# Performance work log

Hardware: AMD Instinct MI355X
Metric: run time of the kernel (lower is better)

The kernel has to match this reference:

```python
import jax, jax.numpy as jnp
import numpy as np

EPS = 1e-12  # F.normalize eps


def setup_inputs() -> dict:
    key = jax.random.key(0)
    ks = jax.random.split(key, 3)
    B, C, D, R = 4096, 32, 128, 8
    return {
        "source": jax.random.normal(ks[0], (B, C, D), dtype=jnp.float32),
        "data": jax.random.normal(ks[1], (B, C, D), dtype=jnp.float32),
        "W": jax.random.normal(ks[2], (R, D, D), dtype=jnp.float32) * (1.0 / np.sqrt(D)),
        "a": jnp.ones((R, C, D), dtype=jnp.float32),
        "c": jnp.ones((R, C, D), dtype=jnp.float32),
        "d": jnp.zeros((R, C, D), dtype=jnp.float32),
    }


def reference(source, data, W, a, c, d):
    # Generate all reflection directions in one batched GEMM:
    # Linear(bias=False): x @ W_r^T, W_r is [out, in]
    v = jnp.einsum("bci,roi->rbco", source, W)          # [R, B, C, D]
    # DynamicTanh: tanh(a*x)*c + d, params [R, C, D] broadcast over batch
    v = jnp.tanh(a[:, None] * v) * c[:, None] + d[:, None]
    # F.normalize(p=2, dim=-1) with eps clamp
    norm = jnp.linalg.norm(v, axis=-1, keepdims=True)
    v = v / jnp.maximum(norm, EPS)

    # Sequential Householder reflections H_R(...H_2(H_1(x)))
    def step(x, vec):
        dot = jnp.sum(vec * x, axis=-1, keepdims=True)  # [B, C, 1]
        return x - 2.0 * vec * dot, None

    out, _ = jax.lax.scan(step, data, v)
    return out
```

## Files before the change

### kernel.cpp

```cpp
#include <hip/hip_runtime.h>
#include <stdint.h>

#define B_DIM 4096
#define C_DIM 32
#define D_DIM 128
#define R_DIM 8
#define BM    128
#define NTHREADS 256

typedef __bf16 bf16x8 __attribute__((ext_vector_type(8)));
typedef float  f32x4  __attribute__((ext_vector_type(4)));

__device__ __forceinline__ uint32_t f2bf(float f) {
  uint32_t u = __float_as_uint(f);
  return (u + 0x7FFFu + ((u >> 16) & 1u)) >> 16;
}

#if __has_builtin(__builtin_amdgcn_exp2f)
#define EXP2F(x) __builtin_amdgcn_exp2f(x)
#else
#define EXP2F(x) exp2f(x)
#endif
#if __has_builtin(__builtin_amdgcn_rcpf)
#define RCPF(x) __builtin_amdgcn_rcpf(x)
#else
#define RCPF(x) (1.0f / (x))
#endif

__device__ __forceinline__ void load_lds16(const void* g, void* l) {
  __builtin_amdgcn_global_load_lds(
      (const __attribute__((address_space(1))) uint32_t*)g,
      (__attribute__((address_space(3))) uint32_t*)l, 16, 0, 0);
}

template <int CTRL>
__device__ __forceinline__ float ror_add(float v) {
  int r = __builtin_amdgcn_update_dpp(0, __builtin_bit_cast(int, v), CTRL, 0xf, 0xf, true);
  return v + __builtin_bit_cast(float, r);
}
__device__ __forceinline__ float red16(float v) {
  v = ror_add<0x128>(v);
  v = ror_add<0x124>(v);
  v = ror_add<0x122>(v);
  v = ror_add<0x121>(v);
  return v;
}

__global__ void prep_w(const float* __restrict__ W, uint32_t* __restrict__ ws) {
  uint32_t t = blockIdx.x * 256u + threadIdx.x;
  uint32_t c  = t >> 2;
  uint32_t j  = t & 3u;
  uint32_t ln = c & 63u;
  uint32_t kt = (c >> 6) & 3u;
  uint32_t n  = (c >> 8) & 7u;
  uint32_t r  = c >> 11;
  uint32_t o  = n * 16u + (ln & 15u);
  uint32_t k  = kt * 32u + (ln >> 4) * 8u + j * 2u;
  const float2 w2 = *reinterpret_cast<const float2*>(
      W + ((size_t)(r * 128u + o)) * 128u + k);
  ws[t] = f2bf(w2.x) | (f2bf(w2.y) << 16);
}

__global__ void prep_acd(const float* __restrict__ A, const float* __restrict__ C,
                         const float* __restrict__ D, float* __restrict__ o) {
  uint32_t t = blockIdx.x * 256u + threadIdx.x;
  uint32_t col = t & 127u, r = (t >> 7) & 7u, c = t >> 10;
  uint32_t in = (r * 32u + c) * 128u + col;
  float av = A[in], cv = C[in], dv = D[in];
  float4 v = make_float4(av * 2.88539008177793f,
                         -2.f * cv, cv + dv, 0.f);
  *reinterpret_cast<float4*>(o + (size_t)t * 4u) = v;
}

__global__ __launch_bounds__(NTHREADS, 2)
void rot_kernel(const float* __restrict__ src, const float* __restrict__ data,
                const uint8_t* __restrict__ wsw, const float* __restrict__ wacd,
                float* __restrict__ out)
{
  __shared__ __align__(16) unsigned char ldsW[65536];

  const uint32_t tid  = threadIdx.x;
  const uint32_t lane = tid & 63u;
  const uint32_t wid  = tid >> 6;
  const uint32_t l15  = lane & 15u;
  const uint32_t lg   = lane >> 4;

  const uint32_t c0     = blockIdx.x & 31u;
  const uint32_t b_base = (blockIdx.x >> 5) * BM;
  const uint32_t rowb   = b_base + wid * 32u;

  {
    #pragma unroll
    for (int j = 0; j < 8; ++j)
      load_lds16(wsw + wid * 1024u + (uint32_t)j * 4096u + lane * 16u,
                 &ldsW[wid * 1024u + (uint32_t)j * 4096u]);
  }

  f32x4 x[2][8];
  #pragma unroll
  for (int rt = 0; rt < 2; ++rt)
    #pragma unroll
    for (int q = 0; q < 4; ++q) {
      const float* xr = data +
          ((size_t)(rowb + rt * 16 + lg * 4 + q) * C_DIM + c0) * D_DIM;
      #pragma unroll
      for (int n = 0; n < 8; ++n) x[rt][n][q] = xr[n * 16 + l15];
    }

  bf16x8 af[2][4];
  #pragma unroll
  for (int rt = 0; rt < 2; ++rt) {
    const float* sr = src +
        ((size_t)(rowb + rt * 16 + l15) * C_DIM + c0) * D_DIM + lg * 8u;
    #pragma unroll
    for (int kt = 0; kt < 4; ++kt) {
      float4 f0 = *reinterpret_cast<const float4*>(sr + kt * 32);
      float4 f1 = *reinterpret_cast<const float4*>(sr + kt * 32 + 4);
      union { uint32_t u[4]; bf16x8 v; } p;
      p.u[0] = f2bf(f0.x) | (f2bf(f0.y) << 16);
      p.u[1] = f2bf(f0.z) | (f2bf(f0.w) << 16);
      p.u[2] = f2bf(f1.x) | (f2bf(f1.y) << 16);
      p.u[3] = f2bf(f1.z) | (f2bf(f1.w) << 16);
      af[rt][kt] = p.v;
    }
  }

  __syncthreads();

  for (int r = 0; r < R_DIM; ++r) {
    f32x4 acd[8];
    {
      const f32x4* g = (const f32x4*)wacd + (uint32_t)(c0 * 8 + r) * 128u + l15;
      #pragma unroll
      for (int n = 0; n < 8; ++n) acd[n] = g[n * 16];
    }
    if (r < 7) {
      const uint8_t* g = wsw + (uint32_t)(r + 1) * 32768u;
      unsigned char* lb = &ldsW[((r + 1) & 1) * 32768u];
      #pragma unroll
      for (int j = 0; j < 8; ++j)
        load_lds16(g + wid * 1024u + (uint32_t)j * 4096u + lane * 16u,
                   &lb[wid * 1024u + (uint32_t)j * 4096u]);
    }

    const uint32_t rb = (r & 1) * 32768u + lane * 16u;
    f32x4 acc[2][8];
    #pragma unroll
    for (int rt = 0; rt < 2; ++rt)
      #pragma unroll
      for (int n = 0; n < 8; ++n) acc[rt][n] = (f32x4){0.f, 0.f, 0.f, 0.f};
    #pragma unroll
    for (int kt = 0; kt < 4; ++kt) {
      #pragma unroll
      for (int n = 0; n < 8; ++n) {
        bf16x8 bq = *reinterpret_cast<const bf16x8*>(
            &ldsW[rb + (uint32_t)((n * 4 + kt) * 1024)]);
        acc[0][n] = __builtin_amdgcn_mfma_f32_16x16x32_bf16(af[0][kt], bq, acc[0][n], 0, 0, 0);
        acc[1][n] = __builtin_amdgcn_mfma_f32_16x16x32_bf16(af[1][kt], bq, acc[1][n], 0, 0, 0);
      }
    }

    f32x4 s2[2] = {{0.f,0.f,0.f,0.f},{0.f,0.f,0.f,0.f}};
    f32x4 tx[2] = {{0.f,0.f,0.f,0.f},{0.f,0.f,0.f,0.f}};
    #pragma unroll
    for (int rt = 0; rt < 2; ++rt) {
      #pragma unroll
      for (int n = 0; n < 8; ++n) {
        float a2 = acd[n][0], m2c = acd[n][1], cdv = acd[n][2];
        f32x4 z = acc[rt][n] * a2;
        f32x4 ep;
        #pragma unroll
        for (int q = 0; q < 4; ++q) ep[q] = EXP2F(z[q]);
        ep = ep + 1.0f;
        f32x4 pr;
        #pragma unroll
        for (int q = 0; q < 4; ++q) pr[q] = RCPF(ep[q]);
        f32x4 t = pr * m2c + cdv;
        acc[rt][n] = t;
        s2[rt] = s2[rt] + t * t;
        tx[rt] = tx[rt] + t * x[rt][n];
      }
    }
    f32x4 sc[2];
    #pragma unroll
    for (int rt = 0; rt < 2; ++rt)
      #pragma unroll
      for (int q = 0; q < 4; ++q) {
        float s = red16(s2[rt][q]);
        float d = red16(tx[rt][q]);
        sc[rt][q] = -2.f * d * RCPF(fmaxf(s, 1e-24f));
      }
    #pragma unroll
    for (int rt = 0; rt < 2; ++rt)
      #pragma unroll
      for (int n = 0; n < 8; ++n)
        x[rt][n] = x[rt][n] + sc[rt] * acc[rt][n];

    __syncthreads();
  }

  #pragma unroll
  for (int rt = 0; rt < 2; ++rt)
    #pragma unroll
    for (int q = 0; q < 4; ++q) {
      float* orow = out +
          ((size_t)(rowb + rt * 16 + lg * 4 + q) * C_DIM + c0) * D_DIM;
      #pragma unroll
      for (int n = 0; n < 8; ++n) orow[n * 16 + l15] = x[rt][n][q];
    }
}

extern "C" void kernel_launch(void* const* d_in, const int* in_sizes, int n_in,
                              void* d_out, int out_size, void* d_ws, size_t ws_size,
                              hipStream_t stream) {
  const float* src  = (const float*)d_in[0];
  const float* data = (const float*)d_in[1];
  const float* W    = (const float*)d_in[2];
  const float* Aa   = (const float*)d_in[3];
  const float* Cc   = (const float*)d_in[4];
  const float* Dd   = (const float*)d_in[5];
  float* out = (float*)d_out;

  uint8_t* wsW  = (uint8_t*)d_ws;
  float*   wacd = (float*)((uint8_t*)d_ws + 262144);

  prep_w<<<dim3(256), dim3(256), 0, stream>>>(W, (uint32_t*)wsW);
  prep_acd<<<dim3(128), dim3(256), 0, stream>>>(Aa, Cc, Dd, wacd);

  dim3 grid((B_DIM / BM) * C_DIM);
  dim3 block(NTHREADS);
  rot_kernel<<<grid, block, 0, stream>>>(src, data, wsW, wacd, out);
}
```

Measured before the change: 97.01 us.

## Single-buffer W in LDS, stage tanh params in LDS, raise occupancy

Cuts the W staging buffer in LDS from double to single buffering. The next reflection's W load is now issued after a barrier that follows the MFMA loop, so it overlaps only the tanh/normalize epilogue. The per-(c,r) a/c/d parameters are split into separate A and MC arrays and preloaded once into LDS, replacing per-iteration global loads. Launch bounds rise to 3 blocks per CU to improve latency hiding, at the cost of an extra barrier per step and less overlap of the W load with the GEMM.

New measurement: 156.6 us. 1.61x slower.

```diff
diff --git a/kernel.cpp b/kernel.cpp
--- a/kernel.cpp
+++ b/kernel.cpp
@@ -62,22 +62,25 @@
 }
 
 __global__ void prep_acd(const float* __restrict__ A, const float* __restrict__ C,
-                         const float* __restrict__ D, float* __restrict__ o) {
+                         const float* __restrict__ D, float* __restrict__ oA,
+                         float2* __restrict__ oMC) {
   uint32_t t = blockIdx.x * 256u + threadIdx.x;
   uint32_t col = t & 127u, r = (t >> 7) & 7u, c = t >> 10;
   uint32_t in = (r * 32u + c) * 128u + col;
   float av = A[in], cv = C[in], dv = D[in];
-  float4 v = make_float4(av * 2.88539008177793f,
-                         -2.f * cv, cv + dv, 0.f);
-  *reinterpret_cast<float4*>(o + (size_t)t * 4u) = v;
-}
-
-__global__ __launch_bounds__(NTHREADS, 2)
+  uint32_t idx = (c * 8u + r) * 128u + col;
+  oA[idx]  = av * 2.88539008177793f;
+  oMC[idx] = make_float2(-2.f * cv, cv + dv);
+}
+
+__global__ __launch_bounds__(NTHREADS, 3)
 void rot_kernel(const float* __restrict__ src, const float* __restrict__ data,
-                const uint8_t* __restrict__ wsw, const float* __restrict__ wacd,
-                float* __restrict__ out)
+                const uint8_t* __restrict__ wsw, const uint8_t* __restrict__ wsA,
+                const uint8_t* __restrict__ wsMC, float* __restrict__ out)
 {
-  __shared__ __align__(16) unsigned char ldsW[65536];
+  __shared__ __align__(16) unsigned char ldsW[32768];
+  __shared__ __align__(16) float  ldsA[8 * 128];
+  __shared__ __align__(16) float2 ldsMC[8 * 128];
 
   const uint32_t tid  = threadIdx.x;
   const uint32_t lane = tid & 63u;
@@ -89,12 +92,16 @@
   const uint32_t b_base = (blockIdx.x >> 5) * BM;
   const uint32_t rowb   = b_base + wid * 32u;
 
-  {
-    #pragma unroll
-    for (int j = 0; j < 8; ++j)
-      load_lds16(wsw + wid * 1024u + (uint32_t)j * 4096u + lane * 16u,
-                 &ldsW[wid * 1024u + (uint32_t)j * 4096u]);
-  }
+  #pragma unroll
+  for (int j = 0; j < 8; ++j)
+    load_lds16(wsw + wid * 1024u + (uint32_t)j * 4096u + lane * 16u,
+               &ldsW[wid * 1024u + (uint32_t)j * 4096u]);
+  load_lds16(wsA + (uint32_t)c0 * 4096u + wid * 1024u + lane * 16u,
+             (uint8_t*)ldsA + wid * 1024u);
+  #pragma unroll
+  for (int j = 0; j < 2; ++j)
+    load_lds16(wsMC + (uint32_t)c0 * 8192u + wid * 1024u + (uint32_t)j * 4096u + lane * 16u,
+               (uint8_t*)ldsMC + wid * 1024u + (uint32_t)j * 4096u);
 
   f32x4 x[2][8];
   #pragma unroll
@@ -128,22 +135,7 @@
   __syncthreads();
 
   for (int r = 0; r < R_DIM; ++r) {
-    f32x4 acd[8];
-    {
-      const f32x4* g = (const f32x4*)wacd + (uint32_t)(c0 * 8 + r) * 128u + l15;
-      #pragma unroll
-      for (int n = 0; n < 8; ++n) acd[n] = g[n * 16];
-    }
-    if (r < 7) {
-      const uint8_t* g = wsw + (uint32_t)(r + 1) * 32768u;
-      unsigned char* lb = &ldsW[((r + 1) & 1) * 32768u];
-      #pragma unroll
-      for (int j = 0; j < 8; ++j)
-        load_lds16(g + wid * 1024u + (uint32_t)j * 4096u + lane * 16u,
-                   &lb[wid * 1024u + (uint32_t)j * 4096u]);
-    }
-
-    const uint32_t rb = (r & 1) * 32768u + lane * 16u;
+    const uint32_t rb = lane * 16u;
     f32x4 acc[2][8];
     #pragma unroll
     for (int rt = 0; rt < 2; ++rt)
@@ -160,13 +152,24 @@
       }
     }
 
+    __syncthreads();
+
+    if (r < 7) {
+      const uint8_t* g = wsw + (uint32_t)(r + 1) * 32768u;
+      #pragma unroll
+      for (int j = 0; j < 8; ++j)
+        load_lds16(g + wid * 1024u + (uint32_t)j * 4096u + lane * 16u,
+                   &ldsW[wid * 1024u + (uint32_t)j * 4096u]);
+    }
+
     f32x4 s2[2] = {{0.f,0.f,0.f,0.f},{0.f,0.f,0.f,0.f}};
     f32x4 tx[2] = {{0.f,0.f,0.f,0.f},{0.f,0.f,0.f,0.f}};
     #pragma unroll
-    for (int rt = 0; rt < 2; ++rt) {
-      #pragma unroll
-      for (int n = 0; n < 8; ++n) {
-        float a2 = acd[n][0], m2c = acd[n][1], cdv = acd[n][2];
+    for (int n = 0; n < 8; ++n) {
+      float  a2 = ldsA [r * 128 + n * 16 + l15];
+      float2 mc = ldsMC[r * 128 + n * 16 + l15];
+      #pragma unroll
+      for (int rt = 0; rt < 2; ++rt) {
         f32x4 z = acc[rt][n] * a2;
         f32x4 ep;
         #pragma unroll
@@ -175,7 +178,7 @@
         f32x4 pr;
         #pragma unroll
         for (int q = 0; q < 4; ++q) pr[q] = RCPF(ep[q]);
-        f32x4 t = pr * m2c + cdv;
+        f32x4 t = pr * mc.x + mc.y;
         acc[rt][n] = t;
         s2[rt] = s2[rt] + t * t;
         tx[rt] = tx[rt] + t * x[rt][n];
@@ -222,12 +225,13 @@
   float* out = (float*)d_out;
 
   uint8_t* wsW  = (uint8_t*)d_ws;
-  float*   wacd = (float*)((uint8_t*)d_ws + 262144);
+  uint8_t* wsA  = wsW + 262144;
+  uint8_t* wsMC = wsA + 131072;
 
   prep_w<<<dim3(256), dim3(256), 0, stream>>>(W, (uint32_t*)wsW);
-  prep_acd<<<dim3(128), dim3(256), 0, stream>>>(Aa, Cc, Dd, wacd);
+  prep_acd<<<dim3(128), dim3(256), 0, stream>>>(Aa, Cc, Dd, (float*)wsA, (float2*)wsMC);
 
   dim3 grid((B_DIM / BM) * C_DIM);
   dim3 block(NTHREADS);
-  rot_kernel<<<grid, block, 0, stream>>>(src, data, wsW, wacd, out);
-}
+  rot_kernel<<<grid, block, 0, stream>>>(src, data, wsW, wsA, wsMC, out);
+}
```

## Load W fragments directly from global memory instead of LDS double-buffering

Applied to the files above, without the earlier changes.

Removes the 64KB LDS double buffer and the async global-to-LDS prefetch of the per-reflection weight matrix. Each wave now reads its bf16 B fragments straight from global memory, relying on L2/L1 caching, which drops the per-iteration __syncthreads barriers. Freeing the LDS may allow more blocks per CU. The cost is more global and L1 traffic and exposed latency on the weight loads before the MFMAs. The epilogue loop order is also swapped so each acd entry is reused across both row tiles.

After: 113.8 us. 17.3% more time.

```diff
diff --git a/kernel.cpp b/kernel.cpp
--- a/kernel.cpp
+++ b/kernel.cpp
@@ -26,12 +26,6 @@
 #else
 #define RCPF(x) (1.0f / (x))
 #endif
-
-__device__ __forceinline__ void load_lds16(const void* g, void* l) {
-  __builtin_amdgcn_global_load_lds(
-      (const __attribute__((address_space(1))) uint32_t*)g,
-      (__attribute__((address_space(3))) uint32_t*)l, 16, 0, 0);
-}
 
 template <int CTRL>
 __device__ __forceinline__ float ror_add(float v) {
@@ -77,24 +71,14 @@
                 const uint8_t* __restrict__ wsw, const float* __restrict__ wacd,
                 float* __restrict__ out)
 {
-  __shared__ __align__(16) unsigned char ldsW[65536];
-
   const uint32_t tid  = threadIdx.x;
   const uint32_t lane = tid & 63u;
   const uint32_t wid  = tid >> 6;
   const uint32_t l15  = lane & 15u;
   const uint32_t lg   = lane >> 4;
 
-  const uint32_t c0     = blockIdx.x & 31u;
-  const uint32_t b_base = (blockIdx.x >> 5) * BM;
-  const uint32_t rowb   = b_base + wid * 32u;
-
-  {
-    #pragma unroll
-    for (int j = 0; j < 8; ++j)
-      load_lds16(wsw + wid * 1024u + (uint32_t)j * 4096u + lane * 16u,
-                 &ldsW[wid * 1024u + (uint32_t)j * 4096u]);
-  }
+  const uint32_t c0   = blockIdx.x & 31u;
+  const uint32_t rowb = (blockIdx.x >> 5) * BM + wid * 32u;
 
   f32x4 x[2][8];
   #pragma unroll
@@ -125,25 +109,16 @@
     }
   }
 
-  __syncthreads();
-
   for (int r = 0; r < R_DIM; ++r) {
     f32x4 acd[8];
     {
-      const f32x4* g = (const f32x4*)wacd + (uint32_t)(c0 * 8 + r) * 128u + l15;
-      #pragma unroll
-      for (int n = 0; n < 8; ++n) acd[n] = g[n * 16];
-    }
-    if (r < 7) {
-      const uint8_t* g = wsw + (uint32_t)(r + 1) * 32768u;
-      unsigned char* lb = &ldsW[((r + 1) & 1) * 32768u];
-      #pragma unroll
-      for (int j = 0; j < 8; ++j)
-        load_lds16(g + wid * 1024u + (uint32_t)j * 4096u + lane * 16u,
-                   &lb[wid * 1024u + (uint32_t)j * 4096u]);
-    }
-
-    const uint32_t rb = (r & 1) * 32768u + lane * 16u;
+      const f32x4* ap = (const f32x4*)wacd + (uint32_t)(c0 * 8 + r) * 128u + l15;
+      #pragma unroll
+      for (int n = 0; n < 8; ++n) acd[n] = ap[n * 16];
+    }
+
+    const bf16x8* wb = reinterpret_cast<const bf16x8*>(
+        wsw + (uint32_t)r * 32768u + lane * 16u);
     f32x4 acc[2][8];
     #pragma unroll
     for (int rt = 0; rt < 2; ++rt)
@@ -151,22 +126,24 @@
       for (int n = 0; n < 8; ++n) acc[rt][n] = (f32x4){0.f, 0.f, 0.f, 0.f};
     #pragma unroll
     for (int kt = 0; kt < 4; ++kt) {
+      bf16x8 bq[8];
+      #pragma unroll
+      for (int n = 0; n < 8; ++n)
+        bq[n] = wb[(uint32_t)(n * 4 + kt) * 64u];
       #pragma unroll
       for (int n = 0; n < 8; ++n) {
-        bf16x8 bq = *reinterpret_cast<const bf16x8*>(
-            &ldsW[rb + (uint32_t)((n * 4 + kt) * 1024)]);
-        acc[0][n] = __builtin_amdgcn_mfma_f32_16x16x32_bf16(af[0][kt], bq, acc[0][n], 0, 0, 0);
-        acc[1][n] = __builtin_amdgcn_mfma_f32_16x16x32_bf16(af[1][kt], bq, acc[1][n], 0, 0, 0);
+        acc[0][n] = __builtin_amdgcn_mfma_f32_16x16x32_bf16(af[0][kt], bq[n], acc[0][n], 0, 0, 0);
+        acc[1][n] = __builtin_amdgcn_mfma_f32_16x16x32_bf16(af[1][kt], bq[n], acc[1][n], 0, 0, 0);
       }
     }
 
     f32x4 s2[2] = {{0.f,0.f,0.f,0.f},{0.f,0.f,0.f,0.f}};
     f32x4 tx[2] = {{0.f,0.f,0.f,0.f},{0.f,0.f,0.f,0.f}};
     #pragma unroll
-    for (int rt = 0; rt < 2; ++rt) {
-      #pragma unroll
-      for (int n = 0; n < 8; ++n) {
-        float a2 = acd[n][0], m2c = acd[n][1], cdv = acd[n][2];
+    for (int n = 0; n < 8; ++n) {
+      float a2 = acd[n][0], m2c = acd[n][1], cdv = acd[n][2];
+      #pragma unroll
+      for (int rt = 0; rt < 2; ++rt) {
         f32x4 z = acc[rt][n] * a2;
         f32x4 ep;
         #pragma unroll
@@ -195,8 +172,6 @@
       #pragma unroll
       for (int n = 0; n < 8; ++n)
         x[rt][n] = x[rt][n] + sc[rt] * acc[rt][n];
-
-    __syncthreads();
   }
 
   #pragma unroll
```
